# Performance work log

Hardware: AMD Instinct MI355X
Metric: run time of the kernel (lower is better)

## Reference

```python
import jax, jax.numpy as jnp
import numpy as np

ALPHA = 0.1
STEPS = 4


def setup_inputs() -> dict:
    key = jax.random.key(0)
    x = jax.random.normal(key, (4, 8192, 1024), dtype=jnp.float32)
    return {"x": x}


def reference(x) -> jnp.ndarray:
    # CtaPostAttnMixer.forward, layout='bld', prefill, steps=4, alpha=0.1
    # Fixed-boundary 1D heat-diffusion stencil along the sequence dim.
    if x.shape[1] < 3:
        return x
    y = x.astype(jnp.float32)
    for _ in range(STEPS):
        # Laplacian on interior tokens: y[l+1] - 2 y[l] + y[l-1]
        lap = y[:, 2:, :] - 2.0 * y[:, 1:-1, :] + y[:, :-2, :]
        y = jnp.concatenate(
            [y[:, :1, :], y[:, 1:-1, :] + ALPHA * lap, y[:, -1:, :]], axis=1
        )
    return y.astype(x.dtype)
```

## Files before the change

kernel.cpp:

```cpp
#include <hip/hip_runtime.h>


namespace {

constexpr int Lr   = 8192;
constexpr int Dq   = 1024 / 4;
constexpr int Bn   = 4;
constexpr int R    = 32;
constexpr int WR   = R + 8;
constexpr int CW   = 64;
constexpr int RT   = Lr / R;
constexpr int CT   = Dq / CW;
constexpr int NXCD = 8;
constexpr int NWG  = RT * CT * Bn;

constexpr float WK0 = 0.4870f;
constexpr float WK1 = 0.2144f;
constexpr float WK2 = 0.0388f;
constexpr float WK3 = 0.0032f;
constexpr float WK4 = 0.0001f;

__device__ __forceinline__ float4 f4_add(float4 a, float4 b) {
    return make_float4(a.x + b.x, a.y + b.y, a.z + b.z, a.w + b.w);
}
__device__ __forceinline__ float4 f4_mul(float s, float4 a) {
    return make_float4(s * a.x, s * a.y, s * a.z, s * a.w);
}
__device__ __forceinline__ float4 f4_fma(float s, float4 a, float4 c) {
    return make_float4(fmaf(s, a.x, c.x), fmaf(s, a.y, c.y),
                       fmaf(s, a.z, c.z), fmaf(s, a.w, c.w));
}

__global__ __launch_bounds__(256, 4)
void mixer4_kernel(const float4* __restrict__ x, float4* __restrict__ y) {
    __shared__ float4 tile[WR][CW];

    const int lin = blockIdx.x;
    const int g   = (lin & (NXCD - 1)) * (NWG / NXCD) + (lin >> 3);
    const int rt  = g & (RT - 1);
    const int bc  = g >> 8;
    const int ct  = bc & (CT - 1);
    const int b   = bc >> 2;
    const int r0  = rt * R;

    const size_t origin = (size_t)b * Lr * Dq + (size_t)ct * CW;
    const float4* __restrict__ xt = x + origin;
    float4* __restrict__       yt = y + origin;

    const int lane = threadIdx.x & 63;
    const int wid  = threadIdx.x >> 6;

#pragma unroll
    for (int ii = 0; ii < WR / 4; ++ii) {
        const int i  = wid + ii * 4;
        int grow = r0 - 4 + i;
        grow = grow < 0 ? 0 : grow;
        grow = grow > Lr - 1 ? Lr - 1 : grow;
        const float4* src = xt + (size_t)grow * Dq + lane;
        __builtin_amdgcn_global_load_lds(
            (const __attribute__((address_space(1))) void*)src,
            (__attribute__((address_space(3))) void*)&tile[i][0],
            16, 0, 0);
    }
    __syncthreads();

    const int kbase = wid * 8;
    float4 win[16];
#pragma unroll
    for (int i = 0; i < 16; ++i) win[i] = tile[kbase + i][lane];

    auto interior = [&](int j) {
        float4 acc = f4_mul(WK0, win[j + 4]);
        acc = f4_fma(WK1, f4_add(win[j + 3], win[j + 5]), acc);
        acc = f4_fma(WK2, f4_add(win[j + 2], win[j + 6]), acc);
        acc = f4_fma(WK3, f4_add(win[j + 1], win[j + 7]), acc);
        acc = f4_fma(WK4, f4_add(win[j + 0], win[j + 8]), acc);
        yt[(size_t)(r0 + kbase + j) * Dq + lane] = acc;
    };

    const bool low  = (r0 == 0)       && (wid == 0);
    const bool high = (r0 == Lr - R)  && (wid == 3);

    if (low) {
        yt[0 * (size_t)Dq + lane] = win[4];
        {
            float4 o = f4_mul(0.2986f, win[4]);
            o = f4_fma(0.4482f, win[5], o);
            o = f4_fma(0.2112f, win[6], o);
            o = f4_fma(0.0387f, win[7], o);
            o = f4_fma(0.0032f, win[8], o);
            o = f4_fma(0.0001f, win[9], o);
            yt[1 * (size_t)Dq + lane] = o;
        }
        {
            float4 o = f4_mul(0.0454f, win[4]);
            o = f4_fma(0.2112f, win[5], o);
            o = f4_fma(0.4869f, win[6], o);
            o = f4_fma(0.2144f, win[7], o);
            o = f4_fma(0.0388f, win[8], o);
            o = f4_fma(0.0032f, win[9], o);
            o = f4_fma(0.0001f, win[10], o);
            yt[2 * (size_t)Dq + lane] = o;
        }
        {
            float4 o = f4_mul(0.0034f, win[4]);
            o = f4_fma(0.0387f, win[5], o);
            o = f4_fma(0.2144f, win[6], o);
            o = f4_fma(0.4870f, win[7], o);
            o = f4_fma(0.2144f, win[8], o);
            o = f4_fma(0.0388f, win[9], o);
            o = f4_fma(0.0032f, win[10], o);
            o = f4_fma(0.0001f, win[11], o);
            yt[3 * (size_t)Dq + lane] = o;
        }
#pragma unroll
        for (int j = 4; j < 8; ++j) interior(j);
    } else if (high) {
#pragma unroll
        for (int j = 0; j < 4; ++j) interior(j);
        yt[(size_t)(Lr - 1) * Dq + lane] = win[11];
        {
            float4 o = f4_mul(0.2986f, win[11]);
            o = f4_fma(0.4482f, win[10], o);
            o = f4_fma(0.2112f, win[9], o);
            o = f4_fma(0.0387f, win[8], o);
            o = f4_fma(0.0032f, win[7], o);
            o = f4_fma(0.0001f, win[6], o);
            yt[(size_t)(Lr - 2) * Dq + lane] = o;
        }
        {
            float4 o = f4_mul(0.0454f, win[11]);
            o = f4_fma(0.2112f, win[10], o);
            o = f4_fma(0.4869f, win[9], o);
            o = f4_fma(0.2144f, win[8], o);
            o = f4_fma(0.0388f, win[7], o);
            o = f4_fma(0.0032f, win[6], o);
            o = f4_fma(0.0001f, win[5], o);
            yt[(size_t)(Lr - 3) * Dq + lane] = o;
        }
        {
            float4 o = f4_mul(0.0034f, win[11]);
            o = f4_fma(0.0387f, win[10], o);
            o = f4_fma(0.2144f, win[9], o);
            o = f4_fma(0.4870f, win[8], o);
            o = f4_fma(0.2144f, win[7], o);
            o = f4_fma(0.0388f, win[6], o);
            o = f4_fma(0.0032f, win[5], o);
            o = f4_fma(0.0001f, win[4], o);
            yt[(size_t)(Lr - 4) * Dq + lane] = o;
        }
    } else {
#pragma unroll
        for (int j = 0; j < 8; ++j) interior(j);
    }
}

}

extern "C" void kernel_launch(void* const* d_in, const int* in_sizes, int n_in,
                              void* d_out, int out_size, void* d_ws, size_t ws_size,
                              hipStream_t stream) {
    const float4* x = (const float4*)d_in[0];
    float4*       y = (float4*)d_out;

    dim3 grid(NWG);
    dim3 block(256);
    hipLaunchKernelGGL(mixer4_kernel, grid, block, 0, stream, x, y);
}
```

Baseline: 228.1 us.

## Loop each workgroup over eight row tiles with double-buffered LDS staging

Each workgroup now handles a strip of eight consecutive row tiles instead of one, which shrinks the grid by eight. The next tile's async global-to-LDS load is issued into an alternate buffer before the current tile is computed. The aim is to overlap load latency with compute and stores, and to cut per-workgroup launch and prologue cost. In exchange, LDS use doubles, launch bounds drop to two blocks per CU, and fewer waves are resident to hide memory latency. The end-of-iteration barrier may also wait on outstanding stores, which would limit the overlap.

After: 237.0 us. 1.04x slower.

```diff
diff --git a/kernel.cpp b/kernel.cpp
--- a/kernel.cpp
+++ b/kernel.cpp
@@ -11,8 +11,9 @@
 constexpr int CW   = 64;
 constexpr int RT   = Lr / R;
 constexpr int CT   = Dq / CW;
+constexpr int MT   = 8;
 constexpr int NXCD = 8;
-constexpr int NWG  = RT * CT * Bn;
+constexpr int NWG  = RT * CT * Bn / MT;
 
 constexpr float WK0 = 0.4870f;
 constexpr float WK1 = 0.2144f;
@@ -31,17 +32,17 @@
                        fmaf(s, a.z, c.z), fmaf(s, a.w, c.w));
 }
 
-__global__ __launch_bounds__(256, 4)
+__global__ __launch_bounds__(256, 2)
 void mixer4_kernel(const float4* __restrict__ x, float4* __restrict__ y) {
-    __shared__ float4 tile[WR][CW];
+    __shared__ float4 buf[2][WR][CW];
 
-    const int lin = blockIdx.x;
-    const int g   = (lin & (NXCD - 1)) * (NWG / NXCD) + (lin >> 3);
-    const int rt  = g & (RT - 1);
-    const int bc  = g >> 8;
-    const int ct  = bc & (CT - 1);
-    const int b   = bc >> 2;
-    const int r0  = rt * R;
+    const int lin   = blockIdx.x;
+    const int g     = (lin & (NXCD - 1)) * (NWG / NXCD) + (lin >> 3);
+    const int strip = g >> 5;
+    const int mrch  = g & 31;
+    const int ct    = strip & (CT - 1);
+    const int b     = strip >> 2;
+    const int rt0   = mrch * MT;
 
     const size_t origin = (size_t)b * Lr * Dq + (size_t)ct * CW;
     const float4* __restrict__ xt = x + origin;
@@ -50,108 +51,122 @@
     const int lane = threadIdx.x & 63;
     const int wid  = threadIdx.x >> 6;
 
+    auto stage = [&](int rt, int sel) {
+        const int r0 = rt * R;
 #pragma unroll
-    for (int ii = 0; ii < WR / 4; ++ii) {
-        const int i  = wid + ii * 4;
-        int grow = r0 - 4 + i;
-        grow = grow < 0 ? 0 : grow;
-        grow = grow > Lr - 1 ? Lr - 1 : grow;
-        const float4* src = xt + (size_t)grow * Dq + lane;
-        __builtin_amdgcn_global_load_lds(
-            (const __attribute__((address_space(1))) void*)src,
-            (__attribute__((address_space(3))) void*)&tile[i][0],
-            16, 0, 0);
-    }
-    __syncthreads();
-
-    const int kbase = wid * 8;
-    float4 win[16];
-#pragma unroll
-    for (int i = 0; i < 16; ++i) win[i] = tile[kbase + i][lane];
-
-    auto interior = [&](int j) {
-        float4 acc = f4_mul(WK0, win[j + 4]);
-        acc = f4_fma(WK1, f4_add(win[j + 3], win[j + 5]), acc);
-        acc = f4_fma(WK2, f4_add(win[j + 2], win[j + 6]), acc);
-        acc = f4_fma(WK3, f4_add(win[j + 1], win[j + 7]), acc);
-        acc = f4_fma(WK4, f4_add(win[j + 0], win[j + 8]), acc);
-        yt[(size_t)(r0 + kbase + j) * Dq + lane] = acc;
+        for (int ii = 0; ii < WR / 4; ++ii) {
+            const int i  = wid + ii * 4;
+            int grow = r0 - 4 + i;
+            grow = grow < 0 ? 0 : grow;
+            grow = grow > Lr - 1 ? Lr - 1 : grow;
+            const float4* src = xt + (size_t)grow * Dq + lane;
+            __builtin_amdgcn_global_load_lds(
+                (const __attribute__((address_space(1))) void*)src,
+                (__attribute__((address_space(3))) void*)&buf[sel][i][0],
+                16, 0, 0);
+        }
     };
 
-    const bool low  = (r0 == 0)       && (wid == 0);
-    const bool high = (r0 == Lr - R)  && (wid == 3);
+    auto compute = [&](int rt, int sel) {
+        const int r0    = rt * R;
+        const int kbase = wid * 8;
+        float4 win[16];
+#pragma unroll
+        for (int i = 0; i < 16; ++i) win[i] = buf[sel][kbase + i][lane];
 
-    if (low) {
-        yt[0 * (size_t)Dq + lane] = win[4];
-        {
-            float4 o = f4_mul(0.2986f, win[4]);
-            o = f4_fma(0.4482f, win[5], o);
-            o = f4_fma(0.2112f, win[6], o);
-            o = f4_fma(0.0387f, win[7], o);
-            o = f4_fma(0.0032f, win[8], o);
-            o = f4_fma(0.0001f, win[9], o);
-            yt[1 * (size_t)Dq + lane] = o;
+        auto interior = [&](int j) {
+            float4 acc = f4_mul(WK0, win[j + 4]);
+            acc = f4_fma(WK1, f4_add(win[j + 3], win[j + 5]), acc);
+            acc = f4_fma(WK2, f4_add(win[j + 2], win[j + 6]), acc);
+            acc = f4_fma(WK3, f4_add(win[j + 1], win[j + 7]), acc);
+            acc = f4_fma(WK4, f4_add(win[j + 0], win[j + 8]), acc);
+            yt[(size_t)(r0 + kbase + j) * Dq + lane] = acc;
+        };
+
+        const bool low  = (rt == 0)      && (wid == 0);
+        const bool high = (rt == RT - 1) && (wid == 3);
+
+        if (low) {
+            yt[0 * (size_t)Dq + lane] = win[4];
+            {
+                float4 o = f4_mul(0.2986f, win[4]);
+                o = f4_fma(0.4482f, win[5], o);
+                o = f4_fma(0.2112f, win[6], o);
+                o = f4_fma(0.0387f, win[7], o);
+                o = f4_fma(0.0032f, win[8], o);
+                o = f4_fma(0.0001f, win[9], o);
+                yt[1 * (size_t)Dq + lane] = o;
+            }
+            {
+                float4 o = f4_mul(0.0454f, win[4]);
+                o = f4_fma(0.2112f, win[5], o);
+                o = f4_fma(0.4869f, win[6], o);
+                o = f4_fma(0.2144f, win[7], o);
+                o = f4_fma(0.0388f, win[8], o);
+                o = f4_fma(0.0032f, win[9], o);
+                o = f4_fma(0.0001f, win[10], o);
+                yt[2 * (size_t)Dq + lane] = o;
+            }
+            {
+                float4 o = f4_mul(0.0034f, win[4]);
+                o = f4_fma(0.0387f, win[5], o);
+                o = f4_fma(0.2144f, win[6], o);
+                o = f4_fma(0.4870f, win[7], o);
+                o = f4_fma(0.2144f, win[8], o);
+                o = f4_fma(0.0388f, win[9], o);
+                o = f4_fma(0.0032f, win[10], o);
+                o = f4_fma(0.0001f, win[11], o);
+                yt[3 * (size_t)Dq + lane] = o;
+            }
+#pragma unroll
+            for (int j = 4; j < 8; ++j) interior(j);
+        } else if (high) {
+#pragma unroll
+            for (int j = 0; j < 4; ++j) interior(j);
+            yt[(size_t)(Lr - 1) * Dq + lane] = win[11];
+            {
+                float4 o = f4_mul(0.2986f, win[11]);
+                o = f4_fma(0.4482f, win[10], o);
+                o = f4_fma(0.2112f, win[9], o);
+                o = f4_fma(0.0387f, win[8], o);
+                o = f4_fma(0.0032f, win[7], o);
+                o = f4_fma(0.0001f, win[6], o);
+                yt[(size_t)(Lr - 2) * Dq + lane] = o;
+            }
+            {
+                float4 o = f4_mul(0.0454f, win[11]);
+                o = f4_fma(0.2112f, win[10], o);
+                o = f4_fma(0.4869f, win[9], o);
+                o = f4_fma(0.2144f, win[8], o);
+                o = f4_fma(0.0388f, win[7], o);
+                o = f4_fma(0.0032f, win[6], o);
+                o = f4_fma(0.0001f, win[5], o);
+                yt[(size_t)(Lr - 3) * Dq + lane] = o;
+            }
+            {
+                float4 o = f4_mul(0.0034f, win[11]);
+                o = f4_fma(0.0387f, win[10], o);
+                o = f4_fma(0.2144f, win[9], o);
+                o = f4_fma(0.4870f, win[8], o);
+                o = f4_fma(0.2144f, win[7], o);
+                o = f4_fma(0.0388f, win[6], o);
+                o = f4_fma(0.0032f, win[5], o);
+                o = f4_fma(0.0001f, win[4], o);
+                yt[(size_t)(Lr - 4) * Dq + lane] = o;
+            }
+        } else {
+#pragma unroll
+            for (int j = 0; j < 8; ++j) interior(j);
         }
-        {
-            float4 o = f4_mul(0.0454f, win[4]);
-            o = f4_fma(0.2112f, win[5], o);
-            o = f4_fma(0.4869f, win[6], o);
-            o = f4_fma(0.2144f, win[7], o);
-            o = f4_fma(0.0388f, win[8], o);
-            o = f4_fma(0.0032f, win[9], o);
-            o = f4_fma(0.0001f, win[10], o);
-            yt[2 * (size_t)Dq + lane] = o;
-        }
-        {
-            float4 o = f4_mul(0.0034f, win[4]);
-            o = f4_fma(0.0387f, win[5], o);
-            o = f4_fma(0.2144f, win[6], o);
-            o = f4_fma(0.4870f, win[7], o);
-            o = f4_fma(0.2144f, win[8], o);
-            o = f4_fma(0.0388f, win[9], o);
-            o = f4_fma(0.0032f, win[10], o);
-            o = f4_fma(0.0001f, win[11], o);
-            yt[3 * (size_t)Dq + lane] = o;
-        }
-#pragma unroll
-        for (int j = 4; j < 8; ++j) interior(j);
-    } else if (high) {
-#pragma unroll
-        for (int j = 0; j < 4; ++j) interior(j);
-        yt[(size_t)(Lr - 1) * Dq + lane] = win[11];
-        {
-            float4 o = f4_mul(0.2986f, win[11]);
-            o = f4_fma(0.4482f, win[10], o);
-            o = f4_fma(0.2112f, win[9], o);
-            o = f4_fma(0.0387f, win[8], o);
-            o = f4_fma(0.0032f, win[7], o);
-            o = f4_fma(0.0001f, win[6], o);
-            yt[(size_t)(Lr - 2) * Dq + lane] = o;
-        }
-        {
-            float4 o = f4_mul(0.0454f, win[11]);
-            o = f4_fma(0.2112f, win[10], o);
-            o = f4_fma(0.4869f, win[9], o);
-            o = f4_fma(0.2144f, win[8], o);
-            o = f4_fma(0.0388f, win[7], o);
-            o = f4_fma(0.0032f, win[6], o);
-            o = f4_fma(0.0001f, win[5], o);
-            yt[(size_t)(Lr - 3) * Dq + lane] = o;
-        }
-        {
-            float4 o = f4_mul(0.0034f, win[11]);
-            o = f4_fma(0.0387f, win[10], o);
-            o = f4_fma(0.2144f, win[9], o);
-            o = f4_fma(0.4870f, win[8], o);
-            o = f4_fma(0.2144f, win[7], o);
-            o = f4_fma(0.0388f, win[6], o);
-            o = f4_fma(0.0032f, win[5], o);
-            o = f4_fma(0.0001f, win[4], o);
-            yt[(size_t)(Lr - 4) * Dq + lane] = o;
-        }
-    } else {
-#pragma unroll
-        for (int j = 0; j < 8; ++j) interior(j);
+    };
+
+    stage(rt0, 0);
+    __syncthreads();
+    for (int t = 0; t < MT; ++t) {
+        const int cur = t & 1;
+        if (t + 1 < MT) stage(rt0 + t + 1, cur ^ 1);
+        compute(rt0 + t, cur);
+        __syncthreads();
     }
 }
 
```
